# Kernel optimization log

Hardware: AMD Instinct MI355X
Metric: run time of the kernel (lower is better)

Reference implementation:

```python
import jax, jax.numpy as jnp
import numpy as np

B, R, E, H = 1024, 1024, 1024, 512
L_ATTR, L_OBJ, L_RELA = 16, 36, 64
EPS = 1e-8


def _lstm_cell(x, h, c, Wih, Whh, bih, bhh):
    # torch.nn.LSTMCell: gates ordered i, f, g, o
    g = x @ Wih.T + bih + h @ Whh.T + bhh
    i, f, gg, o = jnp.split(g, 4, axis=1)
    c2 = jax.nn.sigmoid(f) * c + jax.nn.sigmoid(i) * jnp.tanh(gg)
    h2 = jax.nn.sigmoid(o) * jnp.tanh(c2)
    return h2, c2


def _attend(h, feats, p_feats, mask, Wq, bq, wa, ba):
    att_h = h @ Wq.T + bq                         # [B,H]
    dot = jnp.tanh(p_feats + att_h[:, None, :])   # [B,L,H]
    scores = dot @ wa + ba                        # [B,L]
    w = jax.nn.softmax(scores, axis=1)
    w = w * mask
    w = w / (w.sum(1, keepdims=True) + EPS)
    return jnp.einsum('bl,bld->bd', w, feats)     # [B,R]


def setup_inputs() -> dict:
    key = jax.random.key(0)
    ks = iter(jax.random.split(key, 64))
    n = lambda shp, s=0.02: jax.random.normal(next(ks), shp, dtype=jnp.float32) * s
    inp = {
        'xt': n((B, E), 1.0), 'fc_feats': n((B, R), 1.0),
        'state_h': n((2, B, R), 1.0), 'state_c': n((2, B, R), 1.0),
        'attr_feats': n((B, L_ATTR, R), 1.0), 'obj_feats': n((B, L_OBJ, R), 1.0),
        'rela_feats': n((B, L_RELA, R), 1.0),
        'p_attr_feats': n((B, L_ATTR, H), 1.0), 'p_obj_feats': n((B, L_OBJ, H), 1.0),
        'p_rela_feats': n((B, L_RELA, H), 1.0),
        'attr_masks': jnp.ones((B, L_ATTR), jnp.float32),
        'att_masks': jnp.ones((B, L_OBJ), jnp.float32),
        'rela_masks': jnp.ones((B, L_RELA), jnp.float32),
        'att_Wih': n((4 * R, E + 2 * R)), 'att_Whh': n((4 * R, R)),
        'att_bih': n((4 * R,)), 'att_bhh': n((4 * R,)),
        'lang_Wih': n((4 * R, 4 * R)), 'lang_Whh': n((4 * R, R)),
        'lang_bih': n((4 * R,)), 'lang_bhh': n((4 * R,)),
    }
    for p in ('attr', 'obj', 'rela'):
        inp[p + '_Wq'] = n((H, R)); inp[p + '_bq'] = n((H,))
        inp[p + '_wa'] = n((H,));   inp[p + '_ba'] = n((1,))
    return inp


def reference(xt, fc_feats, state_h, state_c, attr_feats, obj_feats, rela_feats,
              p_attr_feats, p_obj_feats, p_rela_feats, attr_masks, att_masks,
              rela_masks, att_Wih, att_Whh, att_bih, att_bhh, lang_Wih, lang_Whh,
              lang_bih, lang_bhh, attr_Wq, attr_bq, attr_wa, attr_ba, obj_Wq,
              obj_bq, obj_wa, obj_ba, rela_Wq, rela_bq, rela_wa, rela_ba):
    prev_h = state_h[-1]
    att_in = jnp.concatenate([prev_h, fc_feats, xt], axis=1)
    h_att, c_att = _lstm_cell(att_in, state_h[0], state_c[0],
                              att_Wih, att_Whh, att_bih, att_bhh)
    a_attr = _attend(h_att, attr_feats, p_attr_feats, attr_masks,
                     attr_Wq, attr_bq, attr_wa, attr_ba)
    a_obj = _attend(h_att, obj_feats, p_obj_feats, att_masks,
                    obj_Wq, obj_bq, obj_wa, obj_ba)
    a_rela = _attend(h_att, rela_feats, p_rela_feats, rela_masks,
                     rela_Wq, rela_bq, rela_wa, rela_ba)
    lang_in = jnp.concatenate([h_att, a_attr, a_obj, a_rela], axis=1)
    h_lang, c_lang = _lstm_cell(lang_in, state_h[1], state_c[1],
                                lang_Wih, lang_Whh, lang_bih, lang_bhh)
    # dropout in eval mode -> identity
    output = h_lang
    return output, jnp.stack([h_att, h_lang]), jnp.stack([c_att, c_lang])
```

## Files before the change

### kernel.cpp

```cpp
#include <hip/hip_runtime.h>
#include <math.h>

typedef _Float16 half8  __attribute__((ext_vector_type(8)));
typedef _Float16 half4v __attribute__((ext_vector_type(4)));
typedef float    f32x4  __attribute__((ext_vector_type(4)));

__device__ __forceinline__ _Float16 f2h(float f) { return (_Float16)f; }

__device__ __forceinline__ float tanh_fast(float x) {
    float e = __expf(2.f * x);
    return 1.f - 2.f / (e + 1.f);
}

#define LDSB (128 * 40)

__device__ __forceinline__ void gemm_body(
    _Float16* __restrict__ sm,
    const float* A0, const float* A1, const float* A2p, const float* A3,
    const float* A4,
    const float* W0, const float* W1, const float* W2,
    int w0cols, int w0s, int w1s, int nsel,
    _Float16* __restrict__ Cpart, int ldc,
    int kb, int kLen, int ntile, int mtile, int zout)
{
    _Float16* smA = sm;
    _Float16* smW = sm + 2 * LDSB;
    const int tid  = threadIdx.x;
    const int lane = tid & 63;
    const int wid  = tid >> 6;
    const int wm   = wid >> 1, wn = wid & 1;
    const int m0   = mtile * 128;
    const int n0   = ntile * 128;
    const int nt   = kLen >> 5;
    const int srow = tid >> 3;
    const int scol = (tid & 7) << 2;
    const int fr   = lane & 15;
    const int kq   = lane >> 4;

    const float* wsel = nullptr;
    if (nsel) {
        int sel = n0 >> 9;
        const float* Wq = (sel == 0) ? W0 : (sel == 1) ? W1 : W2;
        wsel = Wq + (size_t)((n0 & 511) + srow) * 1024 + kb + scol;
    }

    f32x4 acc[4][4] = {};
    float4 va[4], vw[4];

    auto LOADA = [&](int lk) {
        int gk = kb + lk;
        int seg = gk >> 10;
        const float* ap = (seg == 0) ? A0 : (seg == 1) ? A1 : (seg == 2) ? A2p
                        : (seg == 3) ? A3 : A4;
        ap += (size_t)(m0 + srow) * 1024 + (gk & 1023) + scol;
        #pragma unroll
        for (int p = 0; p < 4; ++p)
            va[p] = *reinterpret_cast<const float4*>(ap + (size_t)p * 32 * 1024);
    };
    auto LOADW = [&](int lk) {
        const float* wp; int wstr;
        if (nsel) {
            wp = wsel + lk; wstr = 1024;
        } else {
            int gk = kb + lk;
            if (gk < w0cols) { wp = W0 + (size_t)(n0 + srow) * w0s + gk + scol;            wstr = w0s; }
            else             { wp = W1 + (size_t)(n0 + srow) * w1s + (gk - w0cols) + scol; wstr = w1s; }
        }
        #pragma unroll
        for (int p = 0; p < 4; ++p)
            vw[p] = *reinterpret_cast<const float4*>(wp + (size_t)p * 32 * wstr);
    };
    auto WRITEA = [&](int buf) {
        _Float16* d = smA + buf * LDSB;
        #pragma unroll
        for (int p = 0; p < 4; ++p) {
            half4v h = { f2h(va[p].x), f2h(va[p].y), f2h(va[p].z), f2h(va[p].w) };
            *reinterpret_cast<half4v*>(&d[(srow + p * 32) * 40 + scol]) = h;
        }
    };
    auto WRITEW = [&](int buf) {
        _Float16* d = smW + buf * LDSB;
        #pragma unroll
        for (int p = 0; p < 4; ++p) {
            half4v h = { f2h(vw[p].x), f2h(vw[p].y), f2h(vw[p].z), f2h(vw[p].w) };
            *reinterpret_cast<half4v*>(&d[(srow + p * 32) * 40 + scol]) = h;
        }
    };
    auto DOMFMA = [&](int buf) {
        half8 af[4], bf[4];
        _Float16* sA = smA + buf * LDSB;
        _Float16* sW = smW + buf * LDSB;
        #pragma unroll
        for (int i = 0; i < 4; ++i) {
            af[i] = *reinterpret_cast<const half8*>(&sA[(wm * 64 + i * 16 + fr) * 40 + kq * 8]);
            bf[i] = *reinterpret_cast<const half8*>(&sW[(wn * 64 + i * 16 + fr) * 40 + kq * 8]);
        }
        #pragma unroll
        for (int i = 0; i < 4; ++i)
            #pragma unroll
            for (int j = 0; j < 4; ++j)
                acc[i][j] = __builtin_amdgcn_mfma_f32_16x16x32_f16(af[i], bf[j], acc[i][j], 0, 0, 0);
    };

    LOADA(0); LOADW(0);
    WRITEA(0); WRITEW(0);
    __syncthreads();
    int cur = 0;
    for (int it = 0; it < nt - 1; ++it) {
        LOADA((it + 1) * 32);
        LOADW((it + 1) * 32);
        DOMFMA(cur);
        WRITEA(cur ^ 1);
        WRITEW(cur ^ 1);
        __syncthreads();
        cur ^= 1;
    }
    DOMFMA(cur);

    _Float16* cp = Cpart + (size_t)zout * 1024ull * (size_t)ldc;
    #pragma unroll
    for (int j = 0; j < 4; ++j) {
        int nc = n0 + wn * 64 + j * 16 + fr;
        #pragma unroll
        for (int i = 0; i < 4; ++i) {
            int rb = m0 + wm * 64 + i * 16 + kq * 4;
            #pragma unroll
            for (int r = 0; r < 4; ++r)
                cp[(size_t)(rb + r) * ldc + nc] = (_Float16)acc[i][j][r];
        }
    }
}

__global__ __launch_bounds__(256) void gemm_hf(
    const float* A0, const float* A1, const float* A2p, const float* A3,
    const float* A4,
    const float* W0, const float* W1, const float* W2,
    int w0cols, int w0s, int w1s, int nsel,
    _Float16* Cpart, int ldc, int kLen, int zbase)
{
    __shared__ _Float16 sm[4 * LDSB];
    gemm_body(sm, A0, A1, A2p, A3, A4, W0, W1, W2, w0cols, w0s, w1s, nsel,
              Cpart, ldc, blockIdx.z * kLen, kLen,
              blockIdx.x, blockIdx.y, zbase + blockIdx.z);
}


__global__ __launch_bounds__(256) void att_scores(
    const float* __restrict__ p_attr, const float* __restrict__ p_obj,
    const float* __restrict__ p_rela,
    const _Float16* __restrict__ q16,
    const float* __restrict__ attr_bq, const float* __restrict__ obj_bq,
    const float* __restrict__ rela_bq,
    const float* __restrict__ attr_wa, const float* __restrict__ obj_wa,
    const float* __restrict__ rela_wa,
    const float* __restrict__ attr_ba, const float* __restrict__ obj_ba,
    const float* __restrict__ rela_ba,
    float* __restrict__ scg)
{
    const unsigned gw = blockIdx.x * 4u + (threadIdx.x >> 6);
    const int lane = threadIdx.x & 63;
    const unsigned b = gw / 116u;
    const int r = (int)(gw - b * 116u);
    const float* pf; const float* bq; const float* wa; const float* ba;
    int l, moff, scoff, L;
    if (r < 16)      { pf = p_attr; bq = attr_bq; wa = attr_wa; ba = attr_ba; l = r;      moff = 0;    scoff = 0;  L = 16; }
    else if (r < 52) { pf = p_obj;  bq = obj_bq;  wa = obj_wa;  ba = obj_ba;  l = r - 16; moff = 512;  scoff = 16; L = 36; }
    else             { pf = p_rela; bq = rela_bq; wa = rela_wa; ba = rela_ba; l = r - 52; moff = 1024; scoff = 52; L = 64; }

    const float4* pf4 = reinterpret_cast<const float4*>(pf) + ((size_t)b * L + l) * 128;
    float4 a0 = pf4[lane];
    float4 a1 = pf4[lane + 64];
    const _Float16* qb = q16 + (size_t)b * 1536 + moff;
    half4v hq0a = *reinterpret_cast<const half4v*>(qb + lane * 4);
    half4v hq0b = *reinterpret_cast<const half4v*>(qb + 256 + lane * 4);
    const _Float16* qb1 = qb + 1536ull * 1024;
    half4v hq1a = *reinterpret_cast<const half4v*>(qb1 + lane * 4);
    half4v hq1b = *reinterpret_cast<const half4v*>(qb1 + 256 + lane * 4);
    const float4* bq4 = reinterpret_cast<const float4*>(bq);
    const float4* wa4 = reinterpret_cast<const float4*>(wa);
    float4 b0 = bq4[lane], b1 = bq4[lane + 64];
    float4 w0 = wa4[lane], w1 = wa4[lane + 64];

    float s = tanh_fast(a0.x + (float)hq0a[0] + (float)hq1a[0] + b0.x) * w0.x
            + tanh_fast(a0.y + (float)hq0a[1] + (float)hq1a[1] + b0.y) * w0.y
            + tanh_fast(a0.z + (float)hq0a[2] + (float)hq1a[2] + b0.z) * w0.z
            + tanh_fast(a0.w + (float)hq0a[3] + (float)hq1a[3] + b0.w) * w0.w
            + tanh_fast(a1.x + (float)hq0b[0] + (float)hq1b[0] + b1.x) * w1.x
            + tanh_fast(a1.y + (float)hq0b[1] + (float)hq1b[1] + b1.y) * w1.y
            + tanh_fast(a1.z + (float)hq0b[2] + (float)hq1b[2] + b1.z) * w1.z
            + tanh_fast(a1.w + (float)hq0b[3] + (float)hq1b[3] + b1.w) * w1.w;
    #pragma unroll
    for (int off = 32; off >= 1; off >>= 1) s += __shfl_xor(s, off);
    if (lane == 0) scg[(size_t)b * 128 + scoff + l] = s + ba[0];
}

template<int L>
__device__ __forceinline__ void wsum_mod(
    const float* __restrict__ feats, const float* __restrict__ scg_b,
    const float* __restrict__ mask_b,
    float* __restrict__ outa, int b, int dhalf, float* wgt)
{
    const int tid = threadIdx.x;
    if (tid < 64) {
        float v = (tid < L) ? scg_b[tid] : -1e30f;
        float m = v;
        #pragma unroll
        for (int off = 32; off >= 1; off >>= 1) m = fmaxf(m, __shfl_xor(m, off));
        float e = (tid < L) ? __expf(v - m) : 0.f;
        float sum = e;
        #pragma unroll
        for (int off = 32; off >= 1; off >>= 1) sum += __shfl_xor(sum, off);
        float w = e / sum;
        float wm = (tid < L) ? w * mask_b[tid] : 0.f;
        float s2 = wm;
        #pragma unroll
        for (int off = 32; off >= 1; off >>= 1) s2 += __shfl_xor(s2, off);
        wgt[tid] = wm / (s2 + 1e-8f);
    }
    __syncthreads();

    const int d0 = dhalf * 512 + tid * 4;
    const float* fp = feats + (size_t)b * L * 1024 + d0;
    f32x4 acc0 = {0.f, 0.f, 0.f, 0.f};
    f32x4 acc1 = {0.f, 0.f, 0.f, 0.f};
    constexpr int NFULL = L / 8;
    #pragma unroll
    for (int g = 0; g < NFULL; ++g) {
        float4 v0 = *reinterpret_cast<const float4*>(fp + (size_t)(g * 8 + 0) * 1024);
        float4 v1 = *reinterpret_cast<const float4*>(fp + (size_t)(g * 8 + 1) * 1024);
        float4 v2 = *reinterpret_cast<const float4*>(fp + (size_t)(g * 8 + 2) * 1024);
        float4 v3 = *reinterpret_cast<const float4*>(fp + (size_t)(g * 8 + 3) * 1024);
        float4 v4 = *reinterpret_cast<const float4*>(fp + (size_t)(g * 8 + 4) * 1024);
        float4 v5 = *reinterpret_cast<const float4*>(fp + (size_t)(g * 8 + 5) * 1024);
        float4 v6 = *reinterpret_cast<const float4*>(fp + (size_t)(g * 8 + 6) * 1024);
        float4 v7 = *reinterpret_cast<const float4*>(fp + (size_t)(g * 8 + 7) * 1024);
        float w0 = wgt[g * 8 + 0], w1 = wgt[g * 8 + 1], w2 = wgt[g * 8 + 2], w3 = wgt[g * 8 + 3];
        float w4 = wgt[g * 8 + 4], w5 = wgt[g * 8 + 5], w6 = wgt[g * 8 + 6], w7 = wgt[g * 8 + 7];
        acc0[0] += w0 * v0.x + w2 * v2.x + w4 * v4.x + w6 * v6.x;
        acc0[1] += w0 * v0.y + w2 * v2.y + w4 * v4.y + w6 * v6.y;
        acc0[2] += w0 * v0.z + w2 * v2.z + w4 * v4.z + w6 * v6.z;
        acc0[3] += w0 * v0.w + w2 * v2.w + w4 * v4.w + w6 * v6.w;
        acc1[0] += w1 * v1.x + w3 * v3.x + w5 * v5.x + w7 * v7.x;
        acc1[1] += w1 * v1.y + w3 * v3.y + w5 * v5.y + w7 * v7.y;
        acc1[2] += w1 * v1.z + w3 * v3.z + w5 * v5.z + w7 * v7.z;
        acc1[3] += w1 * v1.w + w3 * v3.w + w5 * v5.w + w7 * v7.w;
    }
    #pragma unroll
    for (int lg = NFULL * 8; lg < L; lg += 2) {
        float4 v0 = *reinterpret_cast<const float4*>(fp + (size_t)lg * 1024);
        float4 v1 = *reinterpret_cast<const float4*>(fp + (size_t)(lg + 1) * 1024);
        float w0 = wgt[lg], w1 = wgt[lg + 1];
        acc0[0] += w0 * v0.x; acc0[1] += w0 * v0.y; acc0[2] += w0 * v0.z; acc0[3] += w0 * v0.w;
        acc1[0] += w1 * v1.x; acc1[1] += w1 * v1.y; acc1[2] += w1 * v1.z; acc1[3] += w1 * v1.w;
    }
    float4 o;
    o.x = acc0[0] + acc1[0]; o.y = acc0[1] + acc1[1];
    o.z = acc0[2] + acc1[2]; o.w = acc0[3] + acc1[3];
    *reinterpret_cast<float4*>(outa + (size_t)b * 1024 + d0) = o;
}

__global__ __launch_bounds__(128) void att_wsum(
    const float* __restrict__ attr_feats, const float* __restrict__ obj_feats,
    const float* __restrict__ rela_feats,
    const float* __restrict__ attr_masks, const float* __restrict__ att_masks,
    const float* __restrict__ rela_masks,
    const float* __restrict__ scg,
    float* __restrict__ a32)
{
    __shared__ float wgt[64];
    const int bid = blockIdx.x;
    const int sub = bid >> 11;
    const int b   = (bid & 2047) >> 1;
    const int dh  = bid & 1;
    if (sub == 0)
        wsum_mod<64>(rela_feats, scg + (size_t)b * 128 + 52, rela_masks + (size_t)b * 64,
                     a32 + 2ull * 1024 * 1024, b, dh, wgt);
    else if (sub == 1)
        wsum_mod<36>(obj_feats,  scg + (size_t)b * 128 + 16, att_masks + (size_t)b * 36,
                     a32 + 1024ull * 1024, b, dh, wgt);
    else
        wsum_mod<16>(attr_feats, scg + (size_t)b * 128 + 0,  attr_masks + (size_t)b * 16,
                     a32, b, dh, wgt);
}

__global__ __launch_bounds__(256) void lstm4(
    const _Float16* __restrict__ g, size_t zstride, int nz,
    const float* __restrict__ bih, const float* __restrict__ bhh,
    const float* __restrict__ c_prev,
    float* __restrict__ hA, float* __restrict__ hB,
    float* __restrict__ c_out)
{
    int idx = blockIdx.x * 256 + threadIdx.x;
    int b = idx >> 10, r = idx & 1023;
    size_t base = (size_t)b * 4096;
    float gi = bih[r]        + bhh[r];
    float gf = bih[1024 + r] + bhh[1024 + r];
    float gg = bih[2048 + r] + bhh[2048 + r];
    float go = bih[3072 + r] + bhh[3072 + r];
    for (int z = 0; z < nz; ++z) {
        const _Float16* gz = g + (size_t)z * zstride + base;
        gi += (float)gz[r];
        gf += (float)gz[1024 + r];
        gg += (float)gz[2048 + r];
        go += (float)gz[3072 + r];
    }
    float si = 1.f / (1.f + __expf(-gi));
    float sf = 1.f / (1.f + __expf(-gf));
    float so = 1.f / (1.f + __expf(-go));
    float c2 = sf * c_prev[idx] + si * tanh_fast(gg);
    float h2 = so * tanh_fast(c2);
    hA[idx] = h2;
    if (hB) hB[idx] = h2;
    c_out[idx] = c2;
}

extern "C" void kernel_launch(void* const* d_in, const int* in_sizes, int n_in,
                              void* d_out, int out_size, void* d_ws, size_t ws_size,
                              hipStream_t stream)
{
    const size_t BR = 1024ull * 1024ull;
    const float* xt         = (const float*)d_in[0];
    const float* fc         = (const float*)d_in[1];
    const float* state_h    = (const float*)d_in[2];
    const float* state_c    = (const float*)d_in[3];
    const float* attr_feats = (const float*)d_in[4];
    const float* obj_feats  = (const float*)d_in[5];
    const float* rela_feats = (const float*)d_in[6];
    const float* p_attr     = (const float*)d_in[7];
    const float* p_obj      = (const float*)d_in[8];
    const float* p_rela     = (const float*)d_in[9];
    const float* attr_masks = (const float*)d_in[10];
    const float* att_masks  = (const float*)d_in[11];
    const float* rela_masks = (const float*)d_in[12];
    const float* att_Wih    = (const float*)d_in[13];
    const float* att_Whh    = (const float*)d_in[14];
    const float* att_bih    = (const float*)d_in[15];
    const float* att_bhh    = (const float*)d_in[16];
    const float* lang_Wih   = (const float*)d_in[17];
    const float* lang_Whh   = (const float*)d_in[18];
    const float* lang_bih   = (const float*)d_in[19];
    const float* lang_bhh   = (const float*)d_in[20];
    const float* attr_Wq    = (const float*)d_in[21];
    const float* attr_bq    = (const float*)d_in[22];
    const float* attr_wa    = (const float*)d_in[23];
    const float* attr_ba    = (const float*)d_in[24];
    const float* obj_Wq     = (const float*)d_in[25];
    const float* obj_bq     = (const float*)d_in[26];
    const float* obj_wa     = (const float*)d_in[27];
    const float* obj_ba     = (const float*)d_in[28];
    const float* rela_Wq    = (const float*)d_in[29];
    const float* rela_bq    = (const float*)d_in[30];
    const float* rela_wa    = (const float*)d_in[31];
    const float* rela_ba    = (const float*)d_in[32];

    float* out = (float*)d_out;
    const float* h0 = state_h;
    const float* h1 = state_h + BR;
    float* h_att = out + BR;
    float* scg  = out;

    const bool big = ws_size >= 52428800ull;
    const int gslots = big ? 4 : 2;
    _Float16* g16 = (_Float16*)d_ws;
    _Float16* q16 = g16 + (size_t)gslots * 4ull * BR;
    float*    a32 = (float*)(q16 + 2ull * 1536 * 1024);
    float* a_attr = a32;
    float* a_obj  = a32 + BR;
    float* a_rela = a32 + 2 * BR;

    dim3 blk(256);
    const int zsplit = big ? 4 : 2;

    gemm_hf<<<dim3(32, 8, zsplit), blk, 0, stream>>>(
        h1, fc, xt, h0, h0, att_Wih, att_Whh, att_Whh,
        3072, 3072, 1024, 0, g16, 4096, 4096 / zsplit, 0);
    lstm4<<<dim3(4096), blk, 0, stream>>>(
        g16, 4ull * BR, gslots, att_bih, att_bhh, state_c,
        h_att, nullptr, out + 3 * BR);
    gemm_hf<<<dim3(12, 8, 2), blk, 0, stream>>>(
        h_att, h_att, h_att, h_att, h_att,
        attr_Wq, obj_Wq, rela_Wq, 0, 1024, 1024, 1,
        q16, 1536, 512, 0);
    att_scores<<<dim3(29696), blk, 0, stream>>>(
        p_attr, p_obj, p_rela, q16,
        attr_bq, obj_bq, rela_bq, attr_wa, obj_wa, rela_wa,
        attr_ba, obj_ba, rela_ba, scg);
    att_wsum<<<dim3(6144), dim3(128), 0, stream>>>(
        attr_feats, obj_feats, rela_feats,
        attr_masks, att_masks, rela_masks, scg, a32);
    gemm_hf<<<dim3(32, 8, zsplit), blk, 0, stream>>>(
        h_att, a_attr, a_obj, a_rela, h1,
        lang_Wih, lang_Whh, lang_Whh, 4096, 4096, 1024, 0,
        g16, 4096, 5120 / zsplit, 0);
    lstm4<<<dim3(4096), blk, 0, stream>>>(
        g16, 4ull * BR, gslots, lang_bih, lang_bhh, state_c + BR,
        out, out + 2 * BR, out + 4 * BR);
}
```

Measured before the change: 426.1 us.

## Pre-pack weights and activations to tiled fp16 before GEMMs

Adds a pack kernel that converts the LSTM and query weights plus the GEMM input activations into fp16 in a k-block-major tiled layout, then runs a new gemm16 kernel that loads contiguous half8 tiles instead of converting fp32 on the fly. The lstm and weighted-sum kernels now write their outputs straight into the packed fp16 activation buffer. The weights are re-packed on every call, which adds a full read of the fp32 weights and a write of the fp16 copies each launch. This path runs only when the workspace is large enough, otherwise the old path is used.

Result: faster. 373.2 us (-12.4%).

```diff
diff --git a/kernel.cpp b/kernel.cpp
--- a/kernel.cpp
+++ b/kernel.cpp
@@ -12,8 +12,140 @@
     return 1.f - 2.f / (e + 1.f);
 }
 
+__device__ __forceinline__ half8 cvt8(float4 a, float4 b) {
+    half8 h = { f2h(a.x), f2h(a.y), f2h(a.z), f2h(a.w),
+                f2h(b.x), f2h(b.y), f2h(b.z), f2h(b.w) };
+    return h;
+}
+
+__global__ __launch_bounds__(256) void pack_all(
+    const float* __restrict__ att_Wih,  const float* __restrict__ att_Whh,
+    const float* __restrict__ lang_Wih, const float* __restrict__ lang_Whh,
+    const float* __restrict__ attr_Wq,  const float* __restrict__ obj_Wq,
+    const float* __restrict__ rela_Wq,
+    const float* __restrict__ h1, const float* __restrict__ fc,
+    const float* __restrict__ xt, const float* __restrict__ h0,
+    _Float16* __restrict__ attW16, _Float16* __restrict__ langW16,
+    _Float16* __restrict__ qW16,   _Float16* __restrict__ attA16,
+    _Float16* __restrict__ langA16)
+{
+    const int bid = blockIdx.x, tid = threadIdx.x;
+    const float* src; _Float16* dst;
+    if (bid < 8192) {
+        int i = bid * 256 + tid;
+        int row = i / 512, k = (i % 512) * 8;
+        src = (k < 3072) ? att_Wih + (size_t)row * 3072 + k
+                         : att_Whh + (size_t)row * 1024 + (k - 3072);
+        dst = attW16 + ((size_t)(k >> 5) * 4096 + row) * 32 + (k & 31);
+    } else if (bid < 18432) {
+        int i = (bid - 8192) * 256 + tid;
+        int row = i / 640, k = (i % 640) * 8;
+        src = (k < 4096) ? lang_Wih + (size_t)row * 4096 + k
+                         : lang_Whh + (size_t)row * 1024 + (k - 4096);
+        dst = langW16 + ((size_t)(k >> 5) * 4096 + row) * 32 + (k & 31);
+    } else if (bid < 19200) {
+        int i = (bid - 18432) * 256 + tid;
+        int row = i / 128, k = (i % 128) * 8;
+        int m = row >> 9;
+        const float* Wq = (m == 0) ? attr_Wq : (m == 1) ? obj_Wq : rela_Wq;
+        src = Wq + (size_t)(row & 511) * 1024 + k;
+        dst = qW16 + ((size_t)(k >> 5) * 1536 + row) * 32 + (k & 31);
+    } else if (bid < 21248) {
+        int i = (bid - 19200) * 256 + tid;
+        int row = i >> 9, k = (i & 511) * 8;
+        int seg = k >> 10;
+        const float* s = (seg == 0) ? h1 : (seg == 1) ? fc : (seg == 2) ? xt : h0;
+        src = s + (size_t)row * 1024 + (k & 1023);
+        dst = attA16 + ((size_t)(k >> 5) * 1024 + row) * 32 + (k & 31);
+    } else {
+        int i = (bid - 21248) * 256 + tid;
+        int row = i >> 7, k = (i & 127) * 8;
+        src = h1 + (size_t)row * 1024 + k;
+        dst = langA16 + ((size_t)(128 + (k >> 5)) * 1024 + row) * 32 + (k & 31);
+    }
+    float4 v0 = reinterpret_cast<const float4*>(src)[0];
+    float4 v1 = reinterpret_cast<const float4*>(src)[1];
+    *reinterpret_cast<half8*>(dst) = cvt8(v0, v1);
+}
+
+__global__ __launch_bounds__(256) void gemm16(
+    const _Float16* __restrict__ A, int RA,
+    const _Float16* __restrict__ W, int RW,
+    _Float16* __restrict__ Cpart, int ldc, int kLen)
+{
+    __shared__ _Float16 smA[2][128 * 40];
+    __shared__ _Float16 smW[2][128 * 40];
+    const int tid  = threadIdx.x;
+    const int lane = tid & 63;
+    const int wid  = tid >> 6;
+    const int wm   = wid >> 1, wn = wid & 1;
+    const int m0   = blockIdx.y * 128;
+    const int n0   = blockIdx.x * 128;
+    const int kb   = blockIdx.z * kLen;
+    const int nt   = kLen >> 5;
+    const int fr   = lane & 15;
+    const int kq   = lane >> 4;
+    const int r0   = tid >> 2;
+    const int c0   = (tid & 3) * 8;
+
+    f32x4 acc[4][4] = {};
+    half8 va0, va1, vw0, vw1;
+
+    auto LOADP = [&](int lk) {
+        size_t pa = ((size_t)((kb + lk) >> 5) * RA + m0) * 32 + tid * 8;
+        va0 = *reinterpret_cast<const half8*>(A + pa);
+        va1 = *reinterpret_cast<const half8*>(A + pa + 2048);
+        size_t pw = ((size_t)((kb + lk) >> 5) * RW + n0) * 32 + tid * 8;
+        vw0 = *reinterpret_cast<const half8*>(W + pw);
+        vw1 = *reinterpret_cast<const half8*>(W + pw + 2048);
+    };
+    auto WRITE = [&](int buf) {
+        *reinterpret_cast<half8*>(&smA[buf][r0 * 40 + c0])        = va0;
+        *reinterpret_cast<half8*>(&smA[buf][(r0 + 64) * 40 + c0]) = va1;
+        *reinterpret_cast<half8*>(&smW[buf][r0 * 40 + c0])        = vw0;
+        *reinterpret_cast<half8*>(&smW[buf][(r0 + 64) * 40 + c0]) = vw1;
+    };
+    auto DOMFMA = [&](int buf) {
+        half8 af[4], bf[4];
+        #pragma unroll
+        for (int i = 0; i < 4; ++i) {
+            af[i] = *reinterpret_cast<const half8*>(&smA[buf][(wm * 64 + i * 16 + fr) * 40 + kq * 8]);
+            bf[i] = *reinterpret_cast<const half8*>(&smW[buf][(wn * 64 + i * 16 + fr) * 40 + kq * 8]);
+        }
+        #pragma unroll
+        for (int i = 0; i < 4; ++i)
+            #pragma unroll
+            for (int j = 0; j < 4; ++j)
+                acc[i][j] = __builtin_amdgcn_mfma_f32_16x16x32_f16(af[i], bf[j], acc[i][j], 0, 0, 0);
+    };
+
+    LOADP(0); WRITE(0);
+    __syncthreads();
+    int cur = 0;
+    for (int it = 0; it < nt - 1; ++it) {
+        LOADP((it + 1) * 32);
+        DOMFMA(cur);
+        WRITE(cur ^ 1);
+        __syncthreads();
+        cur ^= 1;
+    }
+    DOMFMA(cur);
+
+    _Float16* cp = Cpart + (size_t)blockIdx.z * 1024ull * (size_t)ldc;
+    #pragma unroll
+    for (int j = 0; j < 4; ++j) {
+        int nc = n0 + wn * 64 + j * 16 + fr;
+        #pragma unroll
+        for (int i = 0; i < 4; ++i) {
+            int rb = m0 + wm * 64 + i * 16 + kq * 4;
+            #pragma unroll
+            for (int r = 0; r < 4; ++r)
+                cp[(size_t)(rb + r) * ldc + nc] = (_Float16)acc[i][j][r];
+        }
+    }
+}
+
 #define LDSB (128 * 40)
-
 __device__ __forceinline__ void gemm_body(
     _Float16* __restrict__ sm,
     const float* A0, const float* A1, const float* A2p, const float* A3,
@@ -43,10 +175,8 @@
         const float* Wq = (sel == 0) ? W0 : (sel == 1) ? W1 : W2;
         wsel = Wq + (size_t)((n0 & 511) + srow) * 1024 + kb + scol;
     }
-
     f32x4 acc[4][4] = {};
     float4 va[4], vw[4];
-
     auto LOADA = [&](int lk) {
         int gk = kb + lk;
         int seg = gk >> 10;
@@ -59,9 +189,8 @@
     };
     auto LOADW = [&](int lk) {
         const float* wp; int wstr;
-        if (nsel) {
-            wp = wsel + lk; wstr = 1024;
-        } else {
+        if (nsel) { wp = wsel + lk; wstr = 1024; }
+        else {
             int gk = kb + lk;
             if (gk < w0cols) { wp = W0 + (size_t)(n0 + srow) * w0s + gk + scol;            wstr = w0s; }
             else             { wp = W1 + (size_t)(n0 + srow) * w1s + (gk - w0cols) + scol; wstr = w1s; }
@@ -101,7 +230,6 @@
             for (int j = 0; j < 4; ++j)
                 acc[i][j] = __builtin_amdgcn_mfma_f32_16x16x32_f16(af[i], bf[j], acc[i][j], 0, 0, 0);
     };
-
     LOADA(0); LOADW(0);
     WRITEA(0); WRITEW(0);
     __syncthreads();
@@ -116,7 +244,6 @@
         cur ^= 1;
     }
     DOMFMA(cur);
-
     _Float16* cp = Cpart + (size_t)zout * 1024ull * (size_t)ldc;
     #pragma unroll
     for (int j = 0; j < 4; ++j) {
@@ -143,7 +270,6 @@
               Cpart, ldc, blockIdx.z * kLen, kLen,
               blockIdx.x, blockIdx.y, zbase + blockIdx.z);
 }
-
 
 __global__ __launch_bounds__(256) void att_scores(
     const float* __restrict__ p_attr, const float* __restrict__ p_obj,
@@ -198,7 +324,8 @@
 __device__ __forceinline__ void wsum_mod(
     const float* __restrict__ feats, const float* __restrict__ scg_b,
     const float* __restrict__ mask_b,
-    float* __restrict__ outa, int b, int dhalf, float* wgt)
+    float* __restrict__ outa, _Float16* __restrict__ dst16,
+    int b, int dhalf, float* wgt)
 {
     const int tid = threadIdx.x;
     if (tid < 64) {
@@ -253,10 +380,16 @@
         acc0[0] += w0 * v0.x; acc0[1] += w0 * v0.y; acc0[2] += w0 * v0.z; acc0[3] += w0 * v0.w;
         acc1[0] += w1 * v1.x; acc1[1] += w1 * v1.y; acc1[2] += w1 * v1.z; acc1[3] += w1 * v1.w;
     }
-    float4 o;
-    o.x = acc0[0] + acc1[0]; o.y = acc0[1] + acc1[1];
-    o.z = acc0[2] + acc1[2]; o.w = acc0[3] + acc1[3];
-    *reinterpret_cast<float4*>(outa + (size_t)b * 1024 + d0) = o;
+    float ox = acc0[0] + acc1[0], oy = acc0[1] + acc1[1];
+    float oz = acc0[2] + acc1[2], ow = acc0[3] + acc1[3];
+    if (dst16) {
+        half4v h = { f2h(ox), f2h(oy), f2h(oz), f2h(ow) };
+        *reinterpret_cast<half4v*>(dst16 + ((size_t)(d0 >> 5) * 1024 + b) * 32 + (d0 & 31)) = h;
+    }
+    if (outa) {
+        float4 o; o.x = ox; o.y = oy; o.z = oz; o.w = ow;
+        *reinterpret_cast<float4*>(outa + (size_t)b * 1024 + d0) = o;
+    }
 }
 
 __global__ __launch_bounds__(128) void att_wsum(
@@ -265,7 +398,8 @@
     const float* __restrict__ attr_masks, const float* __restrict__ att_masks,
     const float* __restrict__ rela_masks,
     const float* __restrict__ scg,
-    float* __restrict__ a32)
+    float* __restrict__ a32,
+    _Float16* __restrict__ langA16)
 {
     __shared__ float wgt[64];
     const int bid = blockIdx.x;
@@ -274,13 +408,15 @@
     const int dh  = bid & 1;
     if (sub == 0)
         wsum_mod<64>(rela_feats, scg + (size_t)b * 128 + 52, rela_masks + (size_t)b * 64,
-                     a32 + 2ull * 1024 * 1024, b, dh, wgt);
+                     a32 ? a32 + 2ull * 1024 * 1024 : nullptr,
+                     langA16 ? langA16 + 96ull * 1024 * 32 : nullptr, b, dh, wgt);
     else if (sub == 1)
         wsum_mod<36>(obj_feats,  scg + (size_t)b * 128 + 16, att_masks + (size_t)b * 36,
-                     a32 + 1024ull * 1024, b, dh, wgt);
+                     a32 ? a32 + 1ull * 1024 * 1024 : nullptr,
+                     langA16 ? langA16 + 64ull * 1024 * 32 : nullptr, b, dh, wgt);
     else
         wsum_mod<16>(attr_feats, scg + (size_t)b * 128 + 0,  attr_masks + (size_t)b * 16,
-                     a32, b, dh, wgt);
+                     a32, langA16 ? langA16 + 32ull * 1024 * 32 : nullptr, b, dh, wgt);
 }
 
 __global__ __launch_bounds__(256) void lstm4(
@@ -288,6 +424,7 @@
     const float* __restrict__ bih, const float* __restrict__ bhh,
     const float* __restrict__ c_prev,
     float* __restrict__ hA, float* __restrict__ hB,
+    _Float16* __restrict__ h16,
     float* __restrict__ c_out)
 {
     int idx = blockIdx.x * 256 + threadIdx.x;
@@ -311,6 +448,7 @@
     float h2 = so * tanh_fast(c2);
     hA[idx] = h2;
     if (hB) hB[idx] = h2;
+    if (h16) h16[((size_t)(r >> 5) * 1024 + b) * 32 + (r & 31)] = (_Float16)h2;
     c_out[idx] = c2;
 }
 
@@ -359,6 +497,45 @@
     float* h_att = out + BR;
     float* scg  = out;
 
+    dim3 blk(256);
+
+    const bool pre = ws_size >= 137363456ull;
+    if (pre) {
+        _Float16* g16     = (_Float16*)d_ws;
+        _Float16* q16     = g16     + 16ull * BR;
+        _Float16* attW16  = q16     + 3ull  * BR;
+        _Float16* langW16 = attW16  + 16ull * BR;
+        _Float16* qW16    = langW16 + 20ull * BR;
+        _Float16* attA16  = qW16    + 1536ull * 1024;
+        _Float16* langA16 = attA16  + 4ull  * BR;
+
+        pack_all<<<dim3(21760), blk, 0, stream>>>(
+            att_Wih, att_Whh, lang_Wih, lang_Whh,
+            attr_Wq, obj_Wq, rela_Wq,
+            h1, fc, xt, h0,
+            attW16, langW16, qW16, attA16, langA16);
+        gemm16<<<dim3(32, 8, 4), blk, 0, stream>>>(
+            attA16, 1024, attW16, 4096, g16, 4096, 1024);
+        lstm4<<<dim3(4096), blk, 0, stream>>>(
+            g16, 4ull * BR, 4, att_bih, att_bhh, state_c,
+            h_att, nullptr, langA16, out + 3 * BR);
+        gemm16<<<dim3(12, 8, 2), blk, 0, stream>>>(
+            langA16, 1024, qW16, 1536, q16, 1536, 512);
+        att_scores<<<dim3(29696), blk, 0, stream>>>(
+            p_attr, p_obj, p_rela, q16,
+            attr_bq, obj_bq, rela_bq, attr_wa, obj_wa, rela_wa,
+            attr_ba, obj_ba, rela_ba, scg);
+        att_wsum<<<dim3(6144), dim3(128), 0, stream>>>(
+            attr_feats, obj_feats, rela_feats,
+            attr_masks, att_masks, rela_masks, scg, nullptr, langA16);
+        gemm16<<<dim3(32, 8, 4), blk, 0, stream>>>(
+            langA16, 1024, langW16, 4096, g16, 4096, 1280);
+        lstm4<<<dim3(4096), blk, 0, stream>>>(
+            g16, 4ull * BR, 4, lang_bih, lang_bhh, state_c + BR,
+            out, out + 2 * BR, nullptr, out + 4 * BR);
+        return;
+    }
+
     const bool big = ws_size >= 52428800ull;
     const int gslots = big ? 4 : 2;
     _Float16* g16 = (_Float16*)d_ws;
@@ -367,8 +544,6 @@
     float* a_attr = a32;
     float* a_obj  = a32 + BR;
     float* a_rela = a32 + 2 * BR;
-
-    dim3 blk(256);
     const int zsplit = big ? 4 : 2;
 
     gemm_hf<<<dim3(32, 8, zsplit), blk, 0, stream>>>(
@@ -376,7 +551,7 @@
         3072, 3072, 1024, 0, g16, 4096, 4096 / zsplit, 0);
     lstm4<<<dim3(4096), blk, 0, stream>>>(
         g16, 4ull * BR, gslots, att_bih, att_bhh, state_c,
-        h_att, nullptr, out + 3 * BR);
+        h_att, nullptr, nullptr, out + 3 * BR);
     gemm_hf<<<dim3(12, 8, 2), blk, 0, stream>>>(
         h_att, h_att, h_att, h_att, h_att,
         attr_Wq, obj_Wq, rela_Wq, 0, 1024, 1024, 1,
@@ -387,12 +562,12 @@
         attr_ba, obj_ba, rela_ba, scg);
     att_wsum<<<dim3(6144), dim3(128), 0, stream>>>(
         attr_feats, obj_feats, rela_feats,
-        attr_masks, att_masks, rela_masks, scg, a32);
+        attr_masks, att_masks, rela_masks, scg, a32, nullptr);
     gemm_hf<<<dim3(32, 8, zsplit), blk, 0, stream>>>(
         h_att, a_attr, a_obj, a_rela, h1,
         lang_Wih, lang_Whh, lang_Whh, 4096, 4096, 1024, 0,
         g16, 4096, 5120 / zsplit, 0);
     lstm4<<<dim3(4096), blk, 0, stream>>>(
         g16, 4ull * BR, gslots, lang_bih, lang_bhh, state_c + BR,
-        out, out + 2 * BR, out + 4 * BR);
-}
+        out, out + 2 * BR, nullptr, out + 4 * BR);
+}
```
